# Kernel tuning notes

Measured on AMD Instinct MI355X. Metric: run time of the kernel, lower is better.

## Reference

```python
import jax, jax.numpy as jnp
import numpy as np

NUM_TOKEN = 1024
IN_DIM = 512
OUT_DIM = 512
E = 1024          # expansion_factor * in_token_dims
S = 128
EPS = 1e-5
SQRT_S = float(np.sqrt(S))


def _rope_seq(x):
    """RoPE over axis 1 (sequence), last axis is feature dim. x: [B, L, ..., D]."""
    L = x.shape[1]
    half = x.shape[-1] // 2
    pos = jnp.arange(L, dtype=jnp.float32)
    inv_freq = 10000.0 ** (jnp.arange(half, dtype=jnp.float32) / half)
    sinusoid = pos[:, None] * inv_freq[None, :]          # [L, half]
    bshape = (1, L) + (1,) * (x.ndim - 3) + (half,)
    sin = jnp.sin(sinusoid).reshape(bshape)
    cos = jnp.cos(sinusoid).reshape(bshape)
    x1, x2 = jnp.split(x, 2, axis=-1)
    return jnp.concatenate([x1 * cos - x2 * sin, x2 * cos + x1 * sin], axis=-1)


def setup_inputs() -> dict:
    key = jax.random.key(0)
    ks = jax.random.split(key, 8)
    B = 32
    x = jax.random.normal(ks[0], (B, NUM_TOKEN, IN_DIM), jnp.float32)
    uv_w = jax.random.normal(ks[1], (2 * E + S, IN_DIM), jnp.float32) / np.sqrt(IN_DIM)
    o_w = jax.random.normal(ks[2], (OUT_DIM, E), jnp.float32) / np.sqrt(E)
    gamma = jax.random.uniform(ks[3], (2, S), jnp.float32)
    beta = jax.random.uniform(ks[4], (2, S), jnp.float32)
    w = jax.random.uniform(ks[5], (2 * NUM_TOKEN - 1,), jnp.float32)
    g = jnp.ones((1,), jnp.float32)                       # ScaleNorm gain
    res_scale = jnp.ones((IN_DIM,), jnp.float32)
    layer_scale = jnp.ones((OUT_DIM,), jnp.float32)
    return dict(x=x, uv_w=uv_w, o_w=o_w, gamma=gamma, beta=beta, w=w,
                g=g, res_scale=res_scale, layer_scale=layer_scale)


def reference(x, uv_w, o_w, gamma, beta, w, g, res_scale, layer_scale):
    B, L, D = x.shape
    # ScaleNorm
    norm = jnp.linalg.norm(x, axis=-1, keepdims=True) * (D ** -0.5)
    xn = x / jnp.maximum(norm, EPS) * g
    # shift mixing (time shift: first half channels shifted right by 1 token)
    xs, xp = jnp.split(xn, 2, axis=-1)
    xs = jnp.pad(xs, ((0, 0), (1, 0), (0, 0)))[:, :L, :]
    xn = jnp.concatenate([xs, xp], axis=-1)
    # uv projection + SiLU, then split into u, v, base
    uv = jax.nn.silu(xn @ uv_w.T)                         # [B, L, 2E+S]
    u, v, base = jnp.split(uv, [E, 2 * E], axis=-1)
    # per-head affine then RoPE
    base = base[:, :, None, :] * gamma[None, None] + beta  # [B, L, 2, S]
    base = _rope_seq(base)
    q, k = base[:, :, 0, :], base[:, :, 1, :]
    qk = jnp.einsum('bls,bms->blm', q, k)                 # [B, L, L]
    # structure-mode relative position bias: bias[i, j] = w[j - i + L - 1]
    idx = jnp.arange(L)[None, :] - jnp.arange(L)[:, None] + (L - 1)
    qk = qk + w[idx][None]
    kernel = jnp.square(jax.nn.relu(qk / SQRT_S))
    out = u * jnp.einsum('blm,bme->ble', kernel, v)       # gated quadratic attn
    out = out @ o_w.T                                     # [B, L, OUT_DIM]
    return x * res_scale + out * layer_scale
```

## Files before the change

kernel.cpp:

```cpp
#include <hip/hip_runtime.h>
#include <hip/hip_bf16.h>
#include <math.h>

typedef unsigned short u16;
typedef __bf16 bf16x8 __attribute__((ext_vector_type(8)));
typedef float f32x4 __attribute__((ext_vector_type(4)));
typedef float f32x16 __attribute__((ext_vector_type(16)));

#define NB 32
#define LSEQ 1024
#define DIN 512
#define EDIM 1024
#define SDIM 128
#define NTOK (NB * LSEQ)
#define NUV 2176
#define CHUNK 16

#define AS1 __attribute__((address_space(1)))
#define AS3 __attribute__((address_space(3)))

__device__ __forceinline__ u16 f2bf(float f) {
  unsigned u = __builtin_bit_cast(unsigned, f);
  u += 0x7fffu + ((u >> 16) & 1u);
  return (u16)(u >> 16);
}
__device__ __forceinline__ float bf2f(u16 h) {
  unsigned u = ((unsigned)h) << 16;
  return __builtin_bit_cast(float, u);
}
__device__ __forceinline__ float fast_silu(float x) {
  float t = __builtin_amdgcn_exp2f(-1.44269504088896f * x);
  return x * __builtin_amdgcn_rcpf(1.0f + t);
}


__global__ __launch_bounds__(256) void k_f32_to_bf16(const float* __restrict__ in,
                                                     u16* __restrict__ out, int n4) {
  int i = blockIdx.x * 256 + threadIdx.x;
  if (i < n4) {
    float4 f = ((const float4*)in)[i];
    ushort4 o;
    o.x = f2bf(f.x); o.y = f2bf(f.y); o.z = f2bf(f.z); o.w = f2bf(f.w);
    ((ushort4*)out)[i] = o;
  }
}

__global__ __launch_bounds__(256) void k_normshift(const float* __restrict__ x,
                                                   const float* __restrict__ g,
                                                   u16* __restrict__ xn2) {
  int t = blockIdx.x;
  int l = t & (LSEQ - 1);
  float2 v = ((const float2*)(x + (size_t)t * DIN))[threadIdx.x];
  float ss = v.x * v.x + v.y * v.y;
  for (int o = 32; o > 0; o >>= 1) ss += __shfl_down(ss, o, 64);
  __shared__ float p[4];
  if ((threadIdx.x & 63) == 0) p[threadIdx.x >> 6] = ss;
  __syncthreads();
  float s = p[0] + p[1] + p[2] + p[3];
  float norm = sqrtf(s * (1.0f / (float)DIN));
  float inv = g[0] / fmaxf(norm, 1e-5f);
  int d = threadIdx.x * 2;
  ushort2 ob; ob.x = f2bf(v.x * inv); ob.y = f2bf(v.y * inv);
  if (d >= 256) {
    *(ushort2*)(xn2 + (size_t)t * DIN + d) = ob;
  } else {
    if (l < LSEQ - 1) *(ushort2*)(xn2 + (size_t)(t + 1) * DIN + d) = ob;
    if (l == 0) { ushort2 z = {0, 0}; *(ushort2*)(xn2 + (size_t)t * DIN + d) = z; }
  }
}

__global__ __launch_bounds__(256) void k_rope_table(float* __restrict__ sin_t,
                                                    float* __restrict__ cos_t) {
  int idx = blockIdx.x * 256 + threadIdx.x;
  int l = idx >> 6, j = idx & 63;
  double freq = pow(10000.0, (double)j / 64.0);
  float arg = (float)l * (float)freq;
  double a = (double)arg;
  sin_t[idx] = (float)sin(a);
  cos_t[idx] = (float)cos(a);
}


#define GROW_A(s) (wr * 128 + (s) * 32 + wc * 8)
#define GROW_B(s) (wid * 32 + (s) * 8)

#define STG_PAIR(s, At2, Bt2, dA, dB)                                              \
  do {                                                                             \
    __builtin_amdgcn_global_load_lds(                                              \
        (AS1 unsigned int*)((At2) + (size_t)(GROW_A(s) + srow) * lda + scol),      \
        (AS3 unsigned int*)((dA) + GROW_A(s) * 64), 16, 0, 0);                     \
    __builtin_amdgcn_global_load_lds(                                              \
        (AS1 unsigned int*)((Bt2) + (size_t)(GROW_B(s) + srow) * ldb + scol),      \
        (AS3 unsigned int*)((dB) + GROW_B(s) * 64), 16, 0, 0);                     \
  } while (0)

#define BAR_FENCE()                                                                \
  do { __builtin_amdgcn_s_barrier(); asm volatile("" ::: "memory"); } while (0)


#define RD_A16(dst, cbuf, q)                                                       \
  do {                                                                             \
    _Pragma("unroll") for (int r_ = 0; r_ < 2; ++r_)                               \
    _Pragma("unroll") for (int h_ = 0; h_ < 2; ++h_)                               \
      dst[r_][h_] = *(const bf16x8*)((cbuf) + (wr * 128 + (q) * 32 + r_ * 16 + fr) * 64 + \
                                     (((h_ * 4 + kg) ^ fr7) * 8));                 \
  } while (0)

#define RD_B16(cbuf)                                                               \
  do {                                                                             \
    _Pragma("unroll") for (int n_ = 0; n_ < 4; ++n_)                               \
    _Pragma("unroll") for (int h_ = 0; h_ < 2; ++h_)                               \
      breg[n_][h_] = *(const bf16x8*)((cbuf) + (wc * 64 + n_ * 16 + fr) * 64 +     \
                                      (((h_ * 4 + kg) ^ fr7) * 8));                \
  } while (0)

#define MFMA16T(s, areg)                                                           \
  do {                                                                             \
    __builtin_amdgcn_s_setprio(1);                                                 \
    _Pragma("unroll") for (int r_ = 0; r_ < 2; ++r_)                               \
    _Pragma("unroll") for (int n_ = 0; n_ < 4; ++n_)                               \
    _Pragma("unroll") for (int h_ = 0; h_ < 2; ++h_)                               \
      acc[(s) * 2 + r_][n_] = __builtin_amdgcn_mfma_f32_16x16x32_bf16(             \
          areg[r_][h_], breg[n_][h_], acc[(s) * 2 + r_][n_], 0, 0, 0);             \
    __builtin_amdgcn_s_setprio(0);                                                 \
  } while (0)

#define TILE_STEP16(CA, CB, OA, OB, T)                                             \
  do {                                                                             \
    const bool st_ = ((T) + 2) < nt;                                               \
    const bool more_ = ((T) + 1) < nt;                                             \
    const u16* At2_ = A + (size_t)((T) + 2) * 64;                                  \
    const u16* Bt2_ = B + (size_t)((T) + 2) * 64;                                  \
    MFMA16T(0, ac);                                                                \
    RD_A16(an, CA, 1);                                                             \
    BAR_FENCE();                                                                   \
    if (st_) STG_PAIR(0, At2_, Bt2_, CA, CB);                                      \
    MFMA16T(1, an);                                                                \
    RD_A16(ac, CA, 2);                                                             \
    BAR_FENCE();                                                                   \
    if (st_) STG_PAIR(1, At2_, Bt2_, CA, CB);                                      \
    MFMA16T(2, ac);                                                                \
    RD_A16(an, CA, 3);                                                             \
    BAR_FENCE();                                                                   \
    if (st_) STG_PAIR(2, At2_, Bt2_, CA, CB);                                      \
    MFMA16T(3, an);                                                                \
    if (st_) asm volatile("s_waitcnt vmcnt(6)" ::: "memory");                      \
    else     asm volatile("s_waitcnt vmcnt(0)" ::: "memory");                      \
    BAR_FENCE();                                                                   \
    if (st_) STG_PAIR(3, At2_, Bt2_, CA, CB);                                      \
    if (more_) { RD_B16(OB); RD_A16(ac, OA, 0); }                                  \
  } while (0)

__device__ __forceinline__ void gemm256p16(const u16* __restrict__ A, int lda,
                                           const u16* __restrict__ B, int ldb,
                                           int K, u16* smem, f32x4 (&acc)[8][4]) {
  const int tid = threadIdx.x;
  const int lane = tid & 63, wid = tid >> 6;
  const int wr = wid >> 2, wc = wid & 3;
  const int fr = lane & 15, kg = lane >> 4, fr7 = fr & 7;
  const int srow = lane >> 3;
  const int scol = ((lane & 7) ^ srow) * 8;
  u16* const A0 = smem;
  u16* const B0 = smem + 16384;
  u16* const A1 = smem + 32768;
  u16* const B1 = smem + 49152;
  const int nt = K >> 6;

#pragma unroll
  for (int s = 0; s < 4; ++s) STG_PAIR(s, A, B, A0, B0);
#pragma unroll
  for (int s = 0; s < 4; ++s) STG_PAIR(s, A + 64, B + 64, A1, B1);
  asm volatile("s_waitcnt vmcnt(8)" ::: "memory");
  BAR_FENCE();

  bf16x8 breg[4][2], ac[2][2], an[2][2];
  RD_B16(B0);
  RD_A16(ac, A0, 0);

  for (int tt = 0; tt < nt; tt += 2) {
    TILE_STEP16(A0, B0, A1, B1, tt);
    TILE_STEP16(A1, B1, A0, B0, tt + 1);
  }
}


#define RD_A32(dst, cbuf, q)                                                       \
  do {                                                                             \
    _Pragma("unroll") for (int kk_ = 0; kk_ < 4; ++kk_)                            \
      dst[kk_] = *(const bf16x8*)((cbuf) + (wr * 128 + (q) * 32 + l31) * 64 +      \
                                  (((kk_ * 2 + hi) ^ l7) * 8));                    \
  } while (0)

#define RD_B32(cbuf)                                                               \
  do {                                                                             \
    _Pragma("unroll") for (int np_ = 0; np_ < 2; ++np_)                            \
    _Pragma("unroll") for (int kk_ = 0; kk_ < 4; ++kk_)                            \
      breg[np_][kk_] = *(const bf16x8*)((cbuf) + (wc * 64 + np_ * 32 + l31) * 64 + \
                                        (((kk_ * 2 + hi) ^ l7) * 8));              \
  } while (0)

#define MFMA8(s, areg)                                                             \
  do {                                                                             \
    __builtin_amdgcn_s_setprio(1);                                                 \
    _Pragma("unroll") for (int kk_ = 0; kk_ < 4; ++kk_)                            \
    _Pragma("unroll") for (int np_ = 0; np_ < 2; ++np_)                            \
      acc[s][np_] = __builtin_amdgcn_mfma_f32_32x32x16_bf16(                       \
          areg[kk_], breg[np_][kk_], acc[s][np_], 0, 0, 0);                        \
    __builtin_amdgcn_s_setprio(0);                                                 \
  } while (0)

#define TILE_STEP32(CA, CB, OA, OB, T)                                             \
  do {                                                                             \
    const bool st_ = ((T) + 2) < nt;                                               \
    const bool more_ = ((T) + 1) < nt;                                             \
    const u16* At2_ = A + (size_t)((T) + 2) * 64;                                  \
    const u16* Bt2_ = B + (size_t)((T) + 2) * 64;                                  \
    MFMA8(0, ac);                                                                  \
    RD_A32(an, CA, 1);                                                             \
    BAR_FENCE();                                                                   \
    if (st_) STG_PAIR(0, At2_, Bt2_, CA, CB);                                      \
    MFMA8(1, an);                                                                  \
    RD_A32(ac, CA, 2);                                                             \
    BAR_FENCE();                                                                   \
    if (st_) STG_PAIR(1, At2_, Bt2_, CA, CB);                                      \
    MFMA8(2, ac);                                                                  \
    RD_A32(an, CA, 3);                                                             \
    BAR_FENCE();                                                                   \
    if (st_) STG_PAIR(2, At2_, Bt2_, CA, CB);                                      \
    MFMA8(3, an);                                                                  \
    if (st_) asm volatile("s_waitcnt vmcnt(6)" ::: "memory");                      \
    else     asm volatile("s_waitcnt vmcnt(0)" ::: "memory");                      \
    BAR_FENCE();                                                                   \
    if (st_) STG_PAIR(3, At2_, Bt2_, CA, CB);                                      \
    if (more_) { RD_B32(OB); RD_A32(ac, OA, 0); }                                  \
  } while (0)

__device__ __forceinline__ void gemm256p32(const u16* __restrict__ A, int lda,
                                           const u16* __restrict__ B, int ldb,
                                           int K, u16* smem, f32x16 (&acc)[4][2]) {
  const int tid = threadIdx.x;
  const int lane = tid & 63, wid = tid >> 6;
  const int wr = wid >> 2, wc = wid & 3;
  const int l31 = lane & 31, hi = lane >> 5, l7 = lane & 7;
  const int srow = lane >> 3;
  const int scol = ((lane & 7) ^ srow) * 8;
  u16* const A0 = smem;
  u16* const B0 = smem + 16384;
  u16* const A1 = smem + 32768;
  u16* const B1 = smem + 49152;
  const int nt = K >> 6;

#pragma unroll
  for (int s = 0; s < 4; ++s) STG_PAIR(s, A, B, A0, B0);
#pragma unroll
  for (int s = 0; s < 4; ++s) STG_PAIR(s, A + 64, B + 64, A1, B1);
  asm volatile("s_waitcnt vmcnt(8)" ::: "memory");
  BAR_FENCE();

  bf16x8 breg[2][4], ac[4], an[4];
  RD_B32(B0);
  RD_A32(ac, A0, 0);

  for (int tt = 0; tt < nt; tt += 2) {
    TILE_STEP32(A0, B0, A1, B1, tt);
    TILE_STEP32(A1, B1, A0, B0, tt + 1);
  }
}

__global__ __launch_bounds__(512, 2) void k_gemm_uv(const u16* __restrict__ xn2,
                                                    const u16* __restrict__ wbf,
                                                    u16* __restrict__ u, u16* __restrict__ vt,
                                                    const float* __restrict__ gamma,
                                                    const float* __restrict__ beta,
                                                    const float* __restrict__ sin_t,
                                                    const float* __restrict__ cos_t,
                                                    u16* __restrict__ qout,
                                                    u16* __restrict__ kout) {
  __shared__ __align__(16) u16 smem[65536];
  f32x4 acc[8][4] = {};
  int bid = blockIdx.x;
  int xcd = bid & 7;
  int off = bid >> 3;
  int m0 = (xcd * 16 + off / 9) * 256;
  int n0 = (off % 9) * 256;
  gemm256p16(xn2 + (size_t)m0 * DIN, DIN, wbf + (size_t)n0 * DIN, DIN, DIN, smem, acc);
  int lane = threadIdx.x & 63, wid = threadIdx.x >> 6;
  int wr = wid >> 2, wc = wid & 3;
  int cb = n0 + wc * 64 + (lane & 15);
  int rb = m0 + wr * 128 + (lane >> 4) * 4;
  if (n0 < EDIM) {
#pragma unroll
    for (int mm = 0; mm < 8; ++mm)
#pragma unroll
      for (int n = 0; n < 4; ++n) {
        int c = cb + n * 16;
#pragma unroll
        for (int j = 0; j < 4; ++j) {
          int r = rb + mm * 16 + j;
          u[(size_t)r * EDIM + c] = f2bf(fast_silu(acc[mm][n][j]));
        }
      }
  } else if (n0 < 2 * EDIM) {
    int b = m0 >> 10;
    u16* vtb = vt + (size_t)b * (EDIM * LSEQ);
#pragma unroll
    for (int mm = 0; mm < 8; ++mm) {
      int l0 = (rb + mm * 16) & (LSEQ - 1);
#pragma unroll
      for (int n = 0; n < 4; ++n) {
        int e = cb + n * 16 - EDIM;
        ushort4 o;
        o.x = f2bf(fast_silu(acc[mm][n][0]));
        o.y = f2bf(fast_silu(acc[mm][n][1]));
        o.z = f2bf(fast_silu(acc[mm][n][2]));
        o.w = f2bf(fast_silu(acc[mm][n][3]));
        *(ushort4*)(vtb + (size_t)e * LSEQ + l0) = o;
      }
    }
  } else {
    u16* sbase = smem;
    if (wc < 2) {
#pragma unroll
      for (int mm = 0; mm < 8; ++mm)
#pragma unroll
        for (int n = 0; n < 4; ++n) {
          int c = wc * 64 + (lane & 15) + n * 16;
#pragma unroll
          for (int j = 0; j < 4; ++j) {
            int r = wr * 128 + mm * 16 + (lane >> 4) * 4 + j;
            sbase[r * 136 + c] = f2bf(fast_silu(acc[mm][n][j]));
          }
        }
    }
    __syncthreads();
    int tid = threadIdx.x;
    int j = tid & 63;
    float g0 = gamma[j], g1 = gamma[64 + j], g2 = gamma[128 + j], g3 = gamma[192 + j];
    float e0 = beta[j],  e1 = beta[64 + j],  e2 = beta[128 + j],  e3 = beta[192 + j];
#pragma unroll 4
    for (int i = 0; i < 32; ++i) {
      int row = (tid >> 6) + i * 8;
      int t = m0 + row;
      int l = t & (LSEQ - 1);
      float b1 = bf2f(sbase[row * 136 + j]);
      float b2 = bf2f(sbase[row * 136 + j + 64]);
      float sn = sin_t[l * 64 + j], cs = cos_t[l * 64 + j];
      float y1 = b1 * g0 + e0, y2 = b2 * g1 + e1;
      qout[(size_t)t * SDIM + j]      = f2bf(y1 * cs - y2 * sn);
      qout[(size_t)t * SDIM + j + 64] = f2bf(y2 * cs + y1 * sn);
      y1 = b1 * g2 + e2; y2 = b2 * g3 + e3;
      kout[(size_t)t * SDIM + j]      = f2bf(y1 * cs - y2 * sn);
      kout[(size_t)t * SDIM + j + 64] = f2bf(y2 * cs + y1 * sn);
    }
  }
}


__global__ __launch_bounds__(512, 2) void k_gemm_qk(const u16* __restrict__ q_,
                                                    const u16* __restrict__ k_,
                                                    const float* __restrict__ w,
                                                    u16* __restrict__ scores) {
  __shared__ __align__(16) u16 smem[65536];
  f32x16 acc[4][2] = {};
  int bid = blockIdx.x;
  int xcd = bid & 7;
  int off = bid >> 3;
  int b = xcd * 2 + (off >> 4);
  int t = off & 15;
  int m0 = (t >> 2) * 256, n0 = (t & 3) * 256;
  gemm256p32(q_ + (size_t)(b * LSEQ + m0) * SDIM, SDIM,
             k_ + (size_t)(b * LSEQ + n0) * SDIM, SDIM,
             SDIM, smem, acc);
  int lane = threadIdx.x & 63, wid = threadIdx.x >> 6;
  int wr = wid >> 2, wc = wid & 3;
  int l31 = lane & 31, hi = lane >> 5;
  const float inv_sqrt_s = 0.08838834764831845f;
  u16* sc_b = scores + (size_t)b * LSEQ * LSEQ;
#pragma unroll
  for (int q = 0; q < 4; ++q)
#pragma unroll
    for (int np = 0; np < 2; ++np) {
      int c = n0 + wc * 64 + np * 32 + l31;
#pragma unroll
      for (int g = 0; g < 4; ++g)
#pragma unroll
        for (int j = 0; j < 4; ++j) {
          int r = m0 + wr * 128 + q * 32 + g * 8 + hi * 4 + j;
          float val = (acc[q][np][g * 4 + j] + w[c - r + (LSEQ - 1)]) * inv_sqrt_s;
          val = fmaxf(val, 0.0f);
          sc_b[(size_t)r * LSEQ + c] = f2bf(val * val);
        }
    }
}

__global__ __launch_bounds__(512, 2) void k_gemm_pv(const u16* __restrict__ scores,
                                                    const u16* __restrict__ vt,
                                                    u16* u_io) {
  __shared__ __align__(16) u16 smem[65536];
  f32x16 acc[4][2] = {};
  int bid = blockIdx.x;
  int xcd = bid & 7;
  int off = bid >> 3;
  int b = xcd * 2 + (off >> 4);
  int t = off & 15;
  int m0 = (t >> 2) * 256, n0 = (t & 3) * 256;
  gemm256p32(scores + (size_t)b * LSEQ * LSEQ + (size_t)m0 * LSEQ, LSEQ,
             vt + (size_t)b * LSEQ * EDIM + (size_t)n0 * LSEQ, LSEQ,
             LSEQ, smem, acc);
  int lane = threadIdx.x & 63, wid = threadIdx.x >> 6;
  int wr = wid >> 2, wc = wid & 3;
  int l31 = lane & 31, hi = lane >> 5;
#pragma unroll
  for (int q = 0; q < 4; ++q)
#pragma unroll
    for (int np = 0; np < 2; ++np) {
      int c = n0 + wc * 64 + np * 32 + l31;
#pragma unroll
      for (int g = 0; g < 4; ++g)
#pragma unroll
        for (int j = 0; j < 4; ++j) {
          int r = m0 + wr * 128 + q * 32 + g * 8 + hi * 4 + j;
          size_t idx = (size_t)(b * LSEQ + r) * EDIM + c;
          u_io[idx] = f2bf(acc[q][np][g * 4 + j] * bf2f(u_io[idx]));
        }
    }
}

__global__ __launch_bounds__(512, 2) void k_gemm_out(const u16* __restrict__ attn,
                                                     const u16* __restrict__ owbf,
                                                     const float* __restrict__ x,
                                                     const float* __restrict__ res_scale,
                                                     const float* __restrict__ layer_scale,
                                                     float* __restrict__ out) {
  __shared__ __align__(16) u16 smem[65536];
  f32x16 acc[4][2] = {};
  int bid = blockIdx.x;
  int xcd = bid & 7;
  int off = bid >> 3;
  int m0 = (xcd * 16 + (off >> 1)) * 256;
  int n0 = (off & 1) * 256;
  gemm256p32(attn + (size_t)m0 * EDIM, EDIM, owbf + (size_t)n0 * EDIM, EDIM,
             EDIM, smem, acc);
  int lane = threadIdx.x & 63, wid = threadIdx.x >> 6;
  int wr = wid >> 2, wc = wid & 3;
  int l31 = lane & 31, hi = lane >> 5;
#pragma unroll
  for (int q = 0; q < 4; ++q)
#pragma unroll
    for (int np = 0; np < 2; ++np) {
      int c = n0 + wc * 64 + np * 32 + l31;
#pragma unroll
      for (int g = 0; g < 4; ++g)
#pragma unroll
        for (int j = 0; j < 4; ++j) {
          int r = m0 + wr * 128 + q * 32 + g * 8 + hi * 4 + j;
          out[(size_t)r * DIN + c] =
              x[(size_t)r * DIN + c] * res_scale[c] + acc[q][np][g * 4 + j] * layer_scale[c];
        }
    }
}


extern "C" void kernel_launch(void* const* d_in, const int* in_sizes, int n_in,
                              void* d_out, int out_size, void* d_ws, size_t ws_size,
                              hipStream_t stream) {
  const float* x          = (const float*)d_in[0];
  const float* uv_w       = (const float*)d_in[1];
  const float* o_w        = (const float*)d_in[2];
  const float* gamma      = (const float*)d_in[3];
  const float* beta       = (const float*)d_in[4];
  const float* w          = (const float*)d_in[5];
  const float* g          = (const float*)d_in[6];
  const float* res_scale  = (const float*)d_in[7];
  const float* layer_scale= (const float*)d_in[8];
  float* out = (float*)d_out;

  char* ws = (char*)d_ws;
  u16* xn2    = (u16*)(ws + 0);
  u16* scores = (u16*)(ws + 0);
  u16* q      = (u16*)(ws + 33554432);
  u16* k      = (u16*)(ws + 41943040);
  u16* u_io   = (u16*)(ws + 50331648);
  u16* vt     = (u16*)(ws + 117440512);
  u16* uvw_bf = (u16*)(ws + 184549376);
  u16* ow_bf  = (u16*)(ws + 187170816);
  float* sin_t = (float*)(ws + 188219392);
  float* cos_t = (float*)(ws + 188481536);

  k_f32_to_bf16<<<dim3((NUV * DIN / 4 + 255) / 256), 256, 0, stream>>>(uv_w, uvw_bf, NUV * DIN / 4);
  k_f32_to_bf16<<<dim3((DIN * EDIM / 4 + 255) / 256), 256, 0, stream>>>(o_w, ow_bf, DIN * EDIM / 4);
  k_rope_table<<<dim3(LSEQ * 64 / 256), 256, 0, stream>>>(sin_t, cos_t);
  k_normshift<<<dim3(NTOK), 256, 0, stream>>>(x, g, xn2);

  k_gemm_uv<<<dim3(1152), 512, 0, stream>>>(xn2, uvw_bf, u_io, vt,
                                            gamma, beta, sin_t, cos_t, q, k);

  for (int ch = 0; ch < NB / CHUNK; ++ch) {
    size_t tok0 = (size_t)ch * CHUNK * LSEQ;
    k_gemm_qk<<<dim3(256), 512, 0, stream>>>(q + tok0 * SDIM, k + tok0 * SDIM, w, scores);
    k_gemm_pv<<<dim3(256), 512, 0, stream>>>(scores, vt + tok0 * EDIM, u_io + tok0 * EDIM);
  }

  k_gemm_out<<<dim3(256), 512, 0, stream>>>(u_io, ow_bf, x, res_scale, layer_scale, out);
}
```

Measured before the change: 311.1 us.

## Single-buffer uv GEMM LDS staging to fit more blocks per CU

Replaces the double-buffered LDS pipeline in the uv projection GEMM with a single 64 KB buffer. Each next K-tile is loaded into the same buffer in slices, interleaved with the MFMA sub-steps, and per-slice vmcnt waits keep the data consistent. Shared memory drops from 128 KB to about 66 KB, and the launch bounds ask for more resident blocks per CU so the latency of the in-place refills can be hidden. In exchange, refills now sit on the critical path of the current tile, the tail gets more barriers and waits, and the base-row staging pitch shrinks from 136 to 132 so it fits in the smaller allocation.

```diff
diff --git a/kernel.cpp b/kernel.cpp
--- a/kernel.cpp
+++ b/kernel.cpp
@@ -84,15 +84,17 @@
 #define GROW_A(s) (wr * 128 + (s) * 32 + wc * 8)
 #define GROW_B(s) (wid * 32 + (s) * 8)
 
+#define STG_A1(s, Asrc, dA)                                                        \
+  __builtin_amdgcn_global_load_lds(                                               \
+      (AS1 unsigned int*)((Asrc) + (size_t)(GROW_A(s) + srow) * lda + scol),       \
+      (AS3 unsigned int*)((dA) + GROW_A(s) * 64), 16, 0, 0)
+#define STG_B1(s, Bsrc, dB)                                                        \
+  __builtin_amdgcn_global_load_lds(                                               \
+      (AS1 unsigned int*)((Bsrc) + (size_t)(GROW_B(s) + srow) * ldb + scol),       \
+      (AS3 unsigned int*)((dB) + GROW_B(s) * 64), 16, 0, 0)
+
 #define STG_PAIR(s, At2, Bt2, dA, dB)                                              \
-  do {                                                                             \
-    __builtin_amdgcn_global_load_lds(                                              \
-        (AS1 unsigned int*)((At2) + (size_t)(GROW_A(s) + srow) * lda + scol),      \
-        (AS3 unsigned int*)((dA) + GROW_A(s) * 64), 16, 0, 0);                     \
-    __builtin_amdgcn_global_load_lds(                                              \
-        (AS1 unsigned int*)((Bt2) + (size_t)(GROW_B(s) + srow) * ldb + scol),      \
-        (AS3 unsigned int*)((dB) + GROW_B(s) * 64), 16, 0, 0);                     \
-  } while (0)
+  do { STG_A1(s, At2, dA); STG_B1(s, Bt2, dB); } while (0)
 
 #define BAR_FENCE()                                                                \
   do { __builtin_amdgcn_s_barrier(); asm volatile("" ::: "memory"); } while (0)
@@ -125,33 +127,7 @@
     __builtin_amdgcn_s_setprio(0);                                                 \
   } while (0)
 
-#define TILE_STEP16(CA, CB, OA, OB, T)                                             \
-  do {                                                                             \
-    const bool st_ = ((T) + 2) < nt;                                               \
-    const bool more_ = ((T) + 1) < nt;                                             \
-    const u16* At2_ = A + (size_t)((T) + 2) * 64;                                  \
-    const u16* Bt2_ = B + (size_t)((T) + 2) * 64;                                  \
-    MFMA16T(0, ac);                                                                \
-    RD_A16(an, CA, 1);                                                             \
-    BAR_FENCE();                                                                   \
-    if (st_) STG_PAIR(0, At2_, Bt2_, CA, CB);                                      \
-    MFMA16T(1, an);                                                                \
-    RD_A16(ac, CA, 2);                                                             \
-    BAR_FENCE();                                                                   \
-    if (st_) STG_PAIR(1, At2_, Bt2_, CA, CB);                                      \
-    MFMA16T(2, ac);                                                                \
-    RD_A16(an, CA, 3);                                                             \
-    BAR_FENCE();                                                                   \
-    if (st_) STG_PAIR(2, At2_, Bt2_, CA, CB);                                      \
-    MFMA16T(3, an);                                                                \
-    if (st_) asm volatile("s_waitcnt vmcnt(6)" ::: "memory");                      \
-    else     asm volatile("s_waitcnt vmcnt(0)" ::: "memory");                      \
-    BAR_FENCE();                                                                   \
-    if (st_) STG_PAIR(3, At2_, Bt2_, CA, CB);                                      \
-    if (more_) { RD_B16(OB); RD_A16(ac, OA, 0); }                                  \
-  } while (0)
-
-__device__ __forceinline__ void gemm256p16(const u16* __restrict__ A, int lda,
+__device__ __forceinline__ void gemm256s16(const u16* __restrict__ A, int lda,
                                            const u16* __restrict__ B, int ldb,
                                            int K, u16* smem, f32x4 (&acc)[8][4]) {
   const int tid = threadIdx.x;
@@ -160,26 +136,46 @@
   const int fr = lane & 15, kg = lane >> 4, fr7 = fr & 7;
   const int srow = lane >> 3;
   const int scol = ((lane & 7) ^ srow) * 8;
-  u16* const A0 = smem;
-  u16* const B0 = smem + 16384;
-  u16* const A1 = smem + 32768;
-  u16* const B1 = smem + 49152;
+  u16* const SA = smem;
+  u16* const SB = smem + 16384;
   const int nt = K >> 6;
 
-#pragma unroll
-  for (int s = 0; s < 4; ++s) STG_PAIR(s, A, B, A0, B0);
-#pragma unroll
-  for (int s = 0; s < 4; ++s) STG_PAIR(s, A + 64, B + 64, A1, B1);
-  asm volatile("s_waitcnt vmcnt(8)" ::: "memory");
+  STG_A1(0, A, SA); STG_B1(0, B, SB); STG_B1(1, B, SB);
+  STG_A1(1, A, SA); STG_B1(2, B, SB); STG_B1(3, B, SB);
+  STG_A1(2, A, SA); STG_A1(3, A, SA);
+  asm volatile("s_waitcnt vmcnt(0)" ::: "memory");
+  __builtin_amdgcn_sched_barrier(0);
   BAR_FENCE();
 
   bf16x8 breg[4][2], ac[2][2], an[2][2];
-  RD_B16(B0);
-  RD_A16(ac, A0, 0);
-
-  for (int tt = 0; tt < nt; tt += 2) {
-    TILE_STEP16(A0, B0, A1, B1, tt);
-    TILE_STEP16(A1, B1, A0, B0, tt + 1);
+  RD_B16(SB);
+  RD_A16(ac, SA, 0);
+
+  for (int t = 0; t < nt; ++t) {
+    const bool s1 = (t + 1) < nt;
+    const u16* At1 = A + (size_t)(t + 1) * 64;
+    const u16* Bt1 = B + (size_t)(t + 1) * 64;
+    MFMA16T(0, ac);
+    RD_A16(an, SA, 1);
+    BAR_FENCE();
+    if (s1) { STG_A1(0, At1, SA); STG_B1(0, Bt1, SB); STG_B1(1, Bt1, SB); }
+    MFMA16T(1, an);
+    if (s1) asm volatile("s_waitcnt vmcnt(4)" ::: "memory");
+    else    asm volatile("s_waitcnt vmcnt(1)" ::: "memory");
+    RD_A16(ac, SA, 2);
+    BAR_FENCE();
+    if (s1) { STG_A1(1, At1, SA); STG_B1(2, Bt1, SB); STG_B1(3, Bt1, SB); }
+    MFMA16T(2, ac);
+    if (s1) asm volatile("s_waitcnt vmcnt(6)" ::: "memory");
+    else    asm volatile("s_waitcnt vmcnt(0)" ::: "memory");
+    RD_A16(an, SA, 3);
+    BAR_FENCE();
+    if (s1) STG_A1(2, At1, SA);
+    MFMA16T(3, an);
+    if (s1) asm volatile("s_waitcnt vmcnt(1)" ::: "memory");
+    else    asm volatile("s_waitcnt vmcnt(0)" ::: "memory");
+    BAR_FENCE();
+    if (s1) { STG_A1(3, At1, SA); RD_B16(SB); RD_A16(ac, SA, 0); }
   }
 }
 
@@ -267,7 +263,7 @@
   }
 }
 
-__global__ __launch_bounds__(512, 2) void k_gemm_uv(const u16* __restrict__ xn2,
+__global__ __launch_bounds__(512, 4) void k_gemm_uv(const u16* __restrict__ xn2,
                                                     const u16* __restrict__ wbf,
                                                     u16* __restrict__ u, u16* __restrict__ vt,
                                                     const float* __restrict__ gamma,
@@ -276,14 +272,14 @@
                                                     const float* __restrict__ cos_t,
                                                     u16* __restrict__ qout,
                                                     u16* __restrict__ kout) {
-  __shared__ __align__(16) u16 smem[65536];
+  __shared__ __align__(16) u16 smem[33792];
   f32x4 acc[8][4] = {};
   int bid = blockIdx.x;
   int xcd = bid & 7;
   int off = bid >> 3;
   int m0 = (xcd * 16 + off / 9) * 256;
   int n0 = (off % 9) * 256;
-  gemm256p16(xn2 + (size_t)m0 * DIN, DIN, wbf + (size_t)n0 * DIN, DIN, DIN, smem, acc);
+  gemm256s16(xn2 + (size_t)m0 * DIN, DIN, wbf + (size_t)n0 * DIN, DIN, DIN, smem, acc);
   int lane = threadIdx.x & 63, wid = threadIdx.x >> 6;
   int wr = wid >> 2, wc = wid & 3;
   int cb = n0 + wc * 64 + (lane & 15);
@@ -328,7 +324,7 @@
 #pragma unroll
           for (int j = 0; j < 4; ++j) {
             int r = wr * 128 + mm * 16 + (lane >> 4) * 4 + j;
-            sbase[r * 136 + c] = f2bf(fast_silu(acc[mm][n][j]));
+            sbase[r * 132 + c] = f2bf(fast_silu(acc[mm][n][j]));
           }
         }
     }
@@ -342,8 +338,8 @@
       int row = (tid >> 6) + i * 8;
       int t = m0 + row;
       int l = t & (LSEQ - 1);
-      float b1 = bf2f(sbase[row * 136 + j]);
-      float b2 = bf2f(sbase[row * 136 + j + 64]);
+      float b1 = bf2f(sbase[row * 132 + j]);
+      float b2 = bf2f(sbase[row * 132 + j + 64]);
       float sn = sin_t[l * 64 + j], cs = cos_t[l * 64 + j];
       float y1 = b1 * g0 + e0, y2 = b2 * g1 + e1;
       qout[(size_t)t * SDIM + j]      = f2bf(y1 * cs - y2 * sn);
```

New measurement: 822.2 us. +164.3%, slower.
